# Kernel tuning notes

Hardware: AMD Instinct MI355X
Metric: run time of the kernel (lower is better)

Reference implementation:

```python
import jax, jax.numpy as jnp
import numpy as np

B, S, D, R = 2, 2048, 1024, 224  # batch, seq, n_embd, table_size


def setup_inputs() -> dict:
    key = jax.random.key(0)
    k = jax.random.split(key, 6)
    return {
        "hidden_states": jax.random.normal(k[0], (B, S, D), jnp.float32),
        "w_row": jax.random.normal(k[1], (D, R), jnp.float32) * 0.02,
        "b_row": jnp.zeros((R,), jnp.float32),
        "col_weight": jax.random.normal(k[2], (R, D, R), jnp.float32) * 0.02,
        "col_bias": jnp.zeros((R, R), jnp.float32),
        "target_row_ids": jax.random.randint(k[3], (B, S), 0, R, jnp.int32),
        "target_col_ids": jax.random.randint(k[4], (B, S), 0, R, jnp.int32),
    }


def reference(hidden_states, w_row, b_row, col_weight, col_bias,
              target_row_ids, target_col_ids):
    Bv, Sv, Dv = hidden_states.shape
    Rv = col_bias.shape[0]
    N = Bv * Sv
    hs_flat = hidden_states.reshape(N, Dv)
    r = target_row_ids.reshape(N)
    c = target_col_ids.reshape(N)

    # row loss: standard cross entropy over table_size row logits (mean)
    row_logits = hs_flat @ w_row + b_row                      # [N, R]
    logp_row = jax.nn.log_softmax(row_logits, axis=-1)
    loss_row = -jnp.take_along_axis(logp_row, r[:, None].astype(jnp.int32), axis=1)[:, 0].mean()

    # column loss: per-token row-routed projection + cross entropy (sum / N).
    # Mathematically identical to the original per-row masked loop: each token
    # uses col_weight[row_id] / col_bias[row_id]. We process tokens in fixed-size
    # chunks with lax.scan so FLOPs match the original (N*D*R, not N*R*D*R) and
    # the gathered per-token weights stay bounded in memory.
    CHUNK = 256  # N = 4096 divisible by CHUNK
    hs_c = hs_flat.reshape(N // CHUNK, CHUNK, Dv)
    r_c = r.reshape(N // CHUNK, CHUNK)
    c_c = c.reshape(N // CHUNK, CHUNK)

    def body(acc, xs):
        h, ri, ci = xs                          # [C,D], [C], [C]
        w = col_weight[ri]                      # [C, D, R] irregular gather
        b = col_bias[ri]                        # [C, R]
        logits = jnp.einsum('cd,cdk->ck', h, w) + b
        logp = jax.nn.log_softmax(logits, axis=-1)
        nll = -jnp.take_along_axis(logp, ci[:, None].astype(jnp.int32), axis=1)[:, 0]
        return acc + nll.sum(), None

    loss_col_sum, _ = jax.lax.scan(body, jnp.float32(0.0), (hs_c, r_c, c_c))
    loss_col = loss_col_sum / N
    return loss_row + loss_col
```

## Files before the change

### kernel.cpp

```cpp
#include <hip/hip_runtime.h>
#include <math.h>

#define D_DIM 1024
#define R_DIM 224
#define N_TOK 4096
#define KC 64
#define MT 128
#define NTHREADS 448
#define COL_BLOCKS R_DIM
#define ROW_BLOCKS (N_TOK / MT)
#define GRID (COL_BLOCKS + ROW_BLOCKS)

typedef short bf16x8 __attribute__((ext_vector_type(8)));
typedef short short4_t __attribute__((ext_vector_type(4)));
typedef float floatx4 __attribute__((ext_vector_type(4)));

__device__ __forceinline__ short f2bf(float f) {
    unsigned u = __float_as_uint(f);
    u += 0x7fffu + ((u >> 16) & 1u);
    return (short)(u >> 16);
}

__global__ __launch_bounds__(1024) void sort_kernel(
    const int* __restrict__ rid, int* __restrict__ sorted,
    int* __restrict__ cnt, int* __restrict__ off, float* __restrict__ out)
{
    __shared__ int h[R_DIM];
    __shared__ int cur[R_DIM];
    const int tid = threadIdx.x;
    for (int i = tid; i < R_DIM; i += 1024) h[i] = 0;
    __syncthreads();
    for (int n = tid; n < N_TOK; n += 1024) atomicAdd(&h[rid[n]], 1);
    __syncthreads();
    if (tid == 0) {
        int acc = 0;
        for (int i = 0; i < R_DIM; ++i) {
            cur[i] = acc; off[i] = acc; cnt[i] = h[i]; acc += h[i];
        }
        out[0] = 0.0f;
    }
    __syncthreads();
    for (int n = tid; n < N_TOK; n += 1024) {
        int p = atomicAdd(&cur[rid[n]], 1);
        sorted[p] = n;
    }
}

__global__ __launch_bounds__(NTHREADS) void fused_kernel(
    const float* __restrict__ hs, const float* __restrict__ w_row,
    const float* __restrict__ b_row, const float* __restrict__ w_col,
    const float* __restrict__ b_col, const int* __restrict__ rid,
    const int* __restrict__ cid, const int* __restrict__ sorted,
    const int* __restrict__ cnt, const int* __restrict__ off,
    float* __restrict__ out)
{
    __shared__ short A_sh[MT * KC];
    __shared__ short B_sh[R_DIM * KC];
    __shared__ float Log_sh[16 * R_DIM];
    __shared__ float bias_sh[R_DIM];
    __shared__ int   tok_sh[MT];
    __shared__ float blk_sum;

    const int bid = blockIdx.x;
    const int tid = threadIdx.x;
    const int lane = tid & 63;
    const int wv = tid >> 6;
    const int lm = lane & 15;
    const int lg = lane >> 4;

    const bool is_row = (bid >= COL_BLOCKS);
    const int rho = is_row ? 0 : bid;
    const int tokbase = is_row ? (bid - COL_BLOCKS) * MT : off[rho];
    const int n_tok  = is_row ? MT : cnt[rho];
    const float* W    = is_row ? w_row : (w_col + (size_t)rho * D_DIM * R_DIM);
    const float* bias = is_row ? b_row : (b_col + (size_t)rho * R_DIM);

    if (tid == 0) blk_sum = 0.0f;
    for (int i = tid; i < R_DIM; i += NTHREADS) bias_sh[i] = bias[i];

    char* const Abp = (char*)A_sh;
    char* const Bbp = (char*)B_sh;

    const int n_chunks = (n_tok + MT - 1) / MT;
    for (int p = 0; p < n_chunks; ++p) {
        const int mlim = min(MT, n_tok - p * MT);

        __syncthreads();
        if (tid < MT) {
            int gi = p * MT + tid;
            tok_sh[tid] = (gi < n_tok)
                ? (is_row ? (tokbase + gi) : sorted[tokbase + gi]) : -1;
        }

        floatx4 acc[8][2];
#pragma unroll
        for (int ms = 0; ms < 8; ++ms)
#pragma unroll
            for (int nt = 0; nt < 2; ++nt) acc[ms][nt] = (floatx4)0.0f;

        for (int kc = 0; kc < D_DIM / KC; ++kc) {
            const int K0 = kc * KC;
            __syncthreads();
            for (int i = tid; i < MT * (KC / 4); i += NTHREADS) {
                int row = i >> 4;
                int g = i & 15;
                int tok = tok_sh[row];
                float4 hv = make_float4(0.f, 0.f, 0.f, 0.f);
                if (tok >= 0)
                    hv = *reinterpret_cast<const float4*>(
                        &hs[(size_t)tok * D_DIM + K0 + g * 4]);
                short4_t v = { f2bf(hv.x), f2bf(hv.y), f2bf(hv.z), f2bf(hv.w) };
                *reinterpret_cast<short4_t*>(
                    Abp + row * 128 + ((g * 8) ^ ((row & 7) << 4))) = v;
            }
            for (int i = tid; i < (KC / 4) * (R_DIM / 4); i += NTHREADS) {
                int nq = i % (R_DIM / 4);
                int kq = i / (R_DIM / 4);
                const float* src = W + (size_t)(K0 + kq * 4) * R_DIM + nq * 4;
                float4 r0 = *reinterpret_cast<const float4*>(src);
                float4 r1 = *reinterpret_cast<const float4*>(src + R_DIM);
                float4 r2 = *reinterpret_cast<const float4*>(src + 2 * R_DIM);
                float4 r3 = *reinterpret_cast<const float4*>(src + 3 * R_DIM);
                int n0 = nq * 4;
                short4_t v0 = { f2bf(r0.x), f2bf(r1.x), f2bf(r2.x), f2bf(r3.x) };
                short4_t v1 = { f2bf(r0.y), f2bf(r1.y), f2bf(r2.y), f2bf(r3.y) };
                short4_t v2 = { f2bf(r0.z), f2bf(r1.z), f2bf(r2.z), f2bf(r3.z) };
                short4_t v3 = { f2bf(r0.w), f2bf(r1.w), f2bf(r2.w), f2bf(r3.w) };
                *reinterpret_cast<short4_t*>(Bbp + (n0+0)*128 + ((kq*8) ^ (((n0+0)&7)<<4))) = v0;
                *reinterpret_cast<short4_t*>(Bbp + (n0+1)*128 + ((kq*8) ^ (((n0+1)&7)<<4))) = v1;
                *reinterpret_cast<short4_t*>(Bbp + (n0+2)*128 + ((kq*8) ^ (((n0+2)&7)<<4))) = v2;
                *reinterpret_cast<short4_t*>(Bbp + (n0+3)*128 + ((kq*8) ^ (((n0+3)&7)<<4))) = v3;
            }
            __syncthreads();
#pragma unroll
            for (int ks = 0; ks < 2; ++ks) {
                const int kbyte = ks * 64 + lg * 16;
                bf16x8 b0, b1;
                {
                    int n = wv * 32 + lm;
                    b0 = *reinterpret_cast<const bf16x8*>(
                        Bbp + n * 128 + (kbyte ^ ((n & 7) << 4)));
                    n += 16;
                    b1 = *reinterpret_cast<const bf16x8*>(
                        Bbp + n * 128 + (kbyte ^ ((n & 7) << 4)));
                }
#pragma unroll
                for (int ms = 0; ms < 8; ++ms) {
                    int row = ms * 16 + lm;
                    bf16x8 a = *reinterpret_cast<const bf16x8*>(
                        Abp + row * 128 + (kbyte ^ ((row & 7) << 4)));
                    acc[ms][0] = __builtin_amdgcn_mfma_f32_16x16x32_bf16(
                        a, b0, acc[ms][0], 0, 0, 0);
                    acc[ms][1] = __builtin_amdgcn_mfma_f32_16x16x32_bf16(
                        a, b1, acc[ms][1], 0, 0, 0);
                }
            }
        }

#pragma unroll
        for (int ms = 0; ms < 8; ++ms) {
            __syncthreads();
#pragma unroll
            for (int nt = 0; nt < 2; ++nt) {
                int col = wv * 32 + nt * 16 + lm;
#pragma unroll
                for (int r = 0; r < 4; ++r) {
                    Log_sh[(lg * 4 + r) * R_DIM + col] = acc[ms][nt][r] + bias_sh[col];
                }
            }
            __syncthreads();
            const int mv = mlim - ms * 16;
            for (int rep = 0; rep < 3; ++rep) {
                int t = wv + rep * 7;
                if (t < 16 && t < mv) {
                    float m = -1e30f;
                    for (int c = lane; c < R_DIM; c += 64)
                        m = fmaxf(m, Log_sh[t * R_DIM + c]);
#pragma unroll
                    for (int s = 32; s; s >>= 1) m = fmaxf(m, __shfl_xor(m, s));
                    float sum = 0.0f;
                    for (int c = lane; c < R_DIM; c += 64)
                        sum += __expf(Log_sh[t * R_DIM + c] - m);
#pragma unroll
                    for (int s = 32; s; s >>= 1) sum += __shfl_xor(sum, s);
                    if (lane == 0) {
                        int n = tok_sh[ms * 16 + t];
                        int tgt = is_row ? rid[n] : cid[n];
                        float nll = -(Log_sh[t * R_DIM + tgt] - m - __logf(sum));
                        atomicAdd(&blk_sum, nll);
                    }
                }
            }
        }
    }
    __syncthreads();
    if (tid == 0) atomicAdd(out, blk_sum * (1.0f / N_TOK));
}

extern "C" void kernel_launch(void* const* d_in, const int* in_sizes, int n_in,
                              void* d_out, int out_size, void* d_ws, size_t ws_size,
                              hipStream_t stream)
{
    const float* hs    = (const float*)d_in[0];
    const float* w_row = (const float*)d_in[1];
    const float* b_row = (const float*)d_in[2];
    const float* w_col = (const float*)d_in[3];
    const float* b_col = (const float*)d_in[4];
    const int* rid     = (const int*)d_in[5];
    const int* cid     = (const int*)d_in[6];
    float* out = (float*)d_out;

    int* sorted = (int*)d_ws;
    int* cnt    = sorted + N_TOK;
    int* off    = cnt + R_DIM;

    hipLaunchKernelGGL(sort_kernel, dim3(1), dim3(1024), 0, stream,
                       rid, sorted, cnt, off, out);
    hipLaunchKernelGGL(fused_kernel, dim3(GRID), dim3(NTHREADS), 0, stream,
                       hs, w_row, b_row, w_col, b_col, rid, cid, sorted, cnt, off, out);
}
```

Baseline: 343.7 us.

## Load B fragments directly to registers, skip empty M-tiles, parallel-scan row offsets

Weight fragments are now read from global memory straight into registers in MFMA layout and converted there, with the loads issued before the A-tile barrier, so the B shared-memory staging buffer disappears. MFMAs, A-tile loads and softmax epilogues are skipped for 16-row tiles beyond the bucket's token count, which cuts wasted work for the many small per-row buckets (about 18 tokens each). The A loads are widened to 8 elements, barriers become a raw waitcnt plus s_barrier, and the serial prefix sum in the sort kernel is replaced by a parallel scan. The direct B loads are strided (8 rows per lane, uncoalesced per lane), which may increase global memory transactions.

```diff
diff --git a/kernel.cpp b/kernel.cpp
--- a/kernel.cpp
+++ b/kernel.cpp
@@ -12,7 +12,7 @@
 #define GRID (COL_BLOCKS + ROW_BLOCKS)
 
 typedef short bf16x8 __attribute__((ext_vector_type(8)));
-typedef short short4_t __attribute__((ext_vector_type(4)));
+typedef short short8_t __attribute__((ext_vector_type(8)));
 typedef float floatx4 __attribute__((ext_vector_type(4)));
 
 __device__ __forceinline__ short f2bf(float f) {
@@ -21,24 +21,42 @@
     return (short)(u >> 16);
 }
 
+__device__ __forceinline__ void lds_barrier() {
+    asm volatile("s_waitcnt lgkmcnt(0)" ::: "memory");
+    __builtin_amdgcn_s_barrier();
+}
+
 __global__ __launch_bounds__(1024) void sort_kernel(
     const int* __restrict__ rid, int* __restrict__ sorted,
     int* __restrict__ cnt, int* __restrict__ off, float* __restrict__ out)
 {
-    __shared__ int h[R_DIM];
+    __shared__ int h[256];
+    __shared__ int sc[2][256];
     __shared__ int cur[R_DIM];
     const int tid = threadIdx.x;
-    for (int i = tid; i < R_DIM; i += 1024) h[i] = 0;
+    if (tid < 256) h[tid] = 0;
     __syncthreads();
     for (int n = tid; n < N_TOK; n += 1024) atomicAdd(&h[rid[n]], 1);
     __syncthreads();
-    if (tid == 0) {
-        int acc = 0;
-        for (int i = 0; i < R_DIM; ++i) {
-            cur[i] = acc; off[i] = acc; cnt[i] = h[i]; acc += h[i];
-        }
-        out[0] = 0.0f;
-    }
+    if (tid < 256) sc[0][tid] = h[tid];
+    __syncthreads();
+    int src = 0;
+    for (int d = 1; d < 256; d <<= 1) {
+        if (tid < 256) {
+            int v = sc[src][tid];
+            if (tid >= d) v += sc[src][tid - d];
+            sc[src ^ 1][tid] = v;
+        }
+        __syncthreads();
+        src ^= 1;
+    }
+    if (tid < R_DIM) {
+        int o = sc[src][tid] - h[tid];
+        off[tid] = o;
+        cnt[tid] = h[tid];
+        cur[tid] = o;
+    }
+    if (tid == 0) out[0] = 0.0f;
     __syncthreads();
     for (int n = tid; n < N_TOK; n += 1024) {
         int p = atomicAdd(&cur[rid[n]], 1);
@@ -55,7 +73,6 @@
     float* __restrict__ out)
 {
     __shared__ short A_sh[MT * KC];
-    __shared__ short B_sh[R_DIM * KC];
     __shared__ float Log_sh[16 * R_DIM];
     __shared__ float bias_sh[R_DIM];
     __shared__ int   tok_sh[MT];
@@ -79,13 +96,14 @@
     for (int i = tid; i < R_DIM; i += NTHREADS) bias_sh[i] = bias[i];
 
     char* const Abp = (char*)A_sh;
-    char* const Bbp = (char*)B_sh;
 
     const int n_chunks = (n_tok + MT - 1) / MT;
     for (int p = 0; p < n_chunks; ++p) {
-        const int mlim = min(MT, n_tok - p * MT);
-
-        __syncthreads();
+        const int mlim   = min(MT, n_tok - p * MT);
+        const int mtiles = (mlim + 15) >> 4;
+        const int mrows  = mtiles << 4;
+
+        lds_barrier();
         if (tid < MT) {
             int gi = p * MT + tid;
             tok_sh[tid] = (gi < n_tok)
@@ -100,94 +118,99 @@
 
         for (int kc = 0; kc < D_DIM / KC; ++kc) {
             const int K0 = kc * KC;
-            __syncthreads();
-            for (int i = tid; i < MT * (KC / 4); i += NTHREADS) {
-                int row = i >> 4;
-                int g = i & 15;
+            float braw[2][2][8];
+#pragma unroll
+            for (int ks = 0; ks < 2; ++ks)
+#pragma unroll
+                for (int nt = 0; nt < 2; ++nt) {
+                    const float* bp = W + (size_t)(K0 + ks * 32 + lg * 8) * R_DIM
+                                        + (wv * 32 + nt * 16 + lm);
+#pragma unroll
+                    for (int j = 0; j < 8; ++j) braw[ks][nt][j] = bp[j * R_DIM];
+                }
+
+            lds_barrier();
+            for (int i = tid; i < mrows * (KC / 8); i += NTHREADS) {
+                int row = i >> 3;
+                int g8 = i & 7;
                 int tok = tok_sh[row];
-                float4 hv = make_float4(0.f, 0.f, 0.f, 0.f);
-                if (tok >= 0)
-                    hv = *reinterpret_cast<const float4*>(
-                        &hs[(size_t)tok * D_DIM + K0 + g * 4]);
-                short4_t v = { f2bf(hv.x), f2bf(hv.y), f2bf(hv.z), f2bf(hv.w) };
-                *reinterpret_cast<short4_t*>(
-                    Abp + row * 128 + ((g * 8) ^ ((row & 7) << 4))) = v;
+                float4 h0 = make_float4(0.f, 0.f, 0.f, 0.f);
+                float4 h1 = make_float4(0.f, 0.f, 0.f, 0.f);
+                if (tok >= 0) {
+                    const float* hp = &hs[(size_t)tok * D_DIM + K0 + g8 * 8];
+                    h0 = *reinterpret_cast<const float4*>(hp);
+                    h1 = *reinterpret_cast<const float4*>(hp + 4);
+                }
+                short8_t v = { f2bf(h0.x), f2bf(h0.y), f2bf(h0.z), f2bf(h0.w),
+                               f2bf(h1.x), f2bf(h1.y), f2bf(h1.z), f2bf(h1.w) };
+                *reinterpret_cast<short8_t*>(
+                    Abp + row * 128 + ((g8 * 16) ^ ((row & 7) << 4))) = v;
             }
-            for (int i = tid; i < (KC / 4) * (R_DIM / 4); i += NTHREADS) {
-                int nq = i % (R_DIM / 4);
-                int kq = i / (R_DIM / 4);
-                const float* src = W + (size_t)(K0 + kq * 4) * R_DIM + nq * 4;
-                float4 r0 = *reinterpret_cast<const float4*>(src);
-                float4 r1 = *reinterpret_cast<const float4*>(src + R_DIM);
-                float4 r2 = *reinterpret_cast<const float4*>(src + 2 * R_DIM);
-                float4 r3 = *reinterpret_cast<const float4*>(src + 3 * R_DIM);
-                int n0 = nq * 4;
-                short4_t v0 = { f2bf(r0.x), f2bf(r1.x), f2bf(r2.x), f2bf(r3.x) };
-                short4_t v1 = { f2bf(r0.y), f2bf(r1.y), f2bf(r2.y), f2bf(r3.y) };
-                short4_t v2 = { f2bf(r0.z), f2bf(r1.z), f2bf(r2.z), f2bf(r3.z) };
-                short4_t v3 = { f2bf(r0.w), f2bf(r1.w), f2bf(r2.w), f2bf(r3.w) };
-                *reinterpret_cast<short4_t*>(Bbp + (n0+0)*128 + ((kq*8) ^ (((n0+0)&7)<<4))) = v0;
-                *reinterpret_cast<short4_t*>(Bbp + (n0+1)*128 + ((kq*8) ^ (((n0+1)&7)<<4))) = v1;
-                *reinterpret_cast<short4_t*>(Bbp + (n0+2)*128 + ((kq*8) ^ (((n0+2)&7)<<4))) = v2;
-                *reinterpret_cast<short4_t*>(Bbp + (n0+3)*128 + ((kq*8) ^ (((n0+3)&7)<<4))) = v3;
-            }
-            __syncthreads();
+            lds_barrier();
+
+            bf16x8 bfrag[2][2];
+#pragma unroll
+            for (int ks = 0; ks < 2; ++ks)
+#pragma unroll
+                for (int nt = 0; nt < 2; ++nt) {
+                    bf16x8 v = { f2bf(braw[ks][nt][0]), f2bf(braw[ks][nt][1]),
+                                 f2bf(braw[ks][nt][2]), f2bf(braw[ks][nt][3]),
+                                 f2bf(braw[ks][nt][4]), f2bf(braw[ks][nt][5]),
+                                 f2bf(braw[ks][nt][6]), f2bf(braw[ks][nt][7]) };
+                    bfrag[ks][nt] = v;
+                }
 #pragma unroll
             for (int ks = 0; ks < 2; ++ks) {
                 const int kbyte = ks * 64 + lg * 16;
-                bf16x8 b0, b1;
-                {
-                    int n = wv * 32 + lm;
-                    b0 = *reinterpret_cast<const bf16x8*>(
-                        Bbp + n * 128 + (kbyte ^ ((n & 7) << 4)));
-                    n += 16;
-                    b1 = *reinterpret_cast<const bf16x8*>(
-                        Bbp + n * 128 + (kbyte ^ ((n & 7) << 4)));
-                }
 #pragma unroll
                 for (int ms = 0; ms < 8; ++ms) {
-                    int row = ms * 16 + lm;
-                    bf16x8 a = *reinterpret_cast<const bf16x8*>(
-                        Abp + row * 128 + (kbyte ^ ((row & 7) << 4)));
-                    acc[ms][0] = __builtin_amdgcn_mfma_f32_16x16x32_bf16(
-                        a, b0, acc[ms][0], 0, 0, 0);
-                    acc[ms][1] = __builtin_amdgcn_mfma_f32_16x16x32_bf16(
-                        a, b1, acc[ms][1], 0, 0, 0);
+                    if (ms < mtiles) {
+                        int row = ms * 16 + lm;
+                        bf16x8 a = *reinterpret_cast<const bf16x8*>(
+                            Abp + row * 128 + (kbyte ^ ((row & 7) << 4)));
+                        acc[ms][0] = __builtin_amdgcn_mfma_f32_16x16x32_bf16(
+                            a, bfrag[ks][0], acc[ms][0], 0, 0, 0);
+                        acc[ms][1] = __builtin_amdgcn_mfma_f32_16x16x32_bf16(
+                            a, bfrag[ks][1], acc[ms][1], 0, 0, 0);
+                    }
                 }
             }
         }
 
 #pragma unroll
         for (int ms = 0; ms < 8; ++ms) {
-            __syncthreads();
-#pragma unroll
-            for (int nt = 0; nt < 2; ++nt) {
-                int col = wv * 32 + nt * 16 + lm;
-#pragma unroll
-                for (int r = 0; r < 4; ++r) {
-                    Log_sh[(lg * 4 + r) * R_DIM + col] = acc[ms][nt][r] + bias_sh[col];
-                }
-            }
-            __syncthreads();
-            const int mv = mlim - ms * 16;
-            for (int rep = 0; rep < 3; ++rep) {
-                int t = wv + rep * 7;
-                if (t < 16 && t < mv) {
-                    float m = -1e30f;
-                    for (int c = lane; c < R_DIM; c += 64)
-                        m = fmaxf(m, Log_sh[t * R_DIM + c]);
-#pragma unroll
-                    for (int s = 32; s; s >>= 1) m = fmaxf(m, __shfl_xor(m, s));
-                    float sum = 0.0f;
-                    for (int c = lane; c < R_DIM; c += 64)
-                        sum += __expf(Log_sh[t * R_DIM + c] - m);
-#pragma unroll
-                    for (int s = 32; s; s >>= 1) sum += __shfl_xor(sum, s);
-                    if (lane == 0) {
-                        int n = tok_sh[ms * 16 + t];
-                        int tgt = is_row ? rid[n] : cid[n];
-                        float nll = -(Log_sh[t * R_DIM + tgt] - m - __logf(sum));
-                        atomicAdd(&blk_sum, nll);
+            if (ms < mtiles) {
+                lds_barrier();
+#pragma unroll
+                for (int nt = 0; nt < 2; ++nt) {
+                    int col = wv * 32 + nt * 16 + lm;
+#pragma unroll
+                    for (int r = 0; r < 4; ++r) {
+                        Log_sh[(lg * 4 + r) * R_DIM + col] =
+                            acc[ms][nt][r] + bias_sh[col];
+                    }
+                }
+                lds_barrier();
+                const int mv = mlim - ms * 16;
+                for (int rep = 0; rep < 3; ++rep) {
+                    int t = wv + rep * 7;
+                    if (t < 16 && t < mv) {
+                        float m = -1e30f;
+                        for (int c = lane; c < R_DIM; c += 64)
+                            m = fmaxf(m, Log_sh[t * R_DIM + c]);
+#pragma unroll
+                        for (int s = 32; s; s >>= 1) m = fmaxf(m, __shfl_xor(m, s));
+                        float sum = 0.0f;
+                        for (int c = lane; c < R_DIM; c += 64)
+                            sum += __expf(Log_sh[t * R_DIM + c] - m);
+#pragma unroll
+                        for (int s = 32; s; s >>= 1) sum += __shfl_xor(sum, s);
+                        if (lane == 0) {
+                            int n = tok_sh[ms * 16 + t];
+                            int tgt = is_row ? rid[n] : cid[n];
+                            float nll = -(Log_sh[t * R_DIM + tgt] - m - __logf(sum));
+                            atomicAdd(&blk_sum, nll);
+                        }
                     }
                 }
             }
```

New measurement: 342.1 us. No clear change (-0.5%).
